# Performance work log

Hardware: AMD Instinct MI355X
Metric: run time of the kernel (lower is better)

The kernel has to match this reference:

```python
import jax, jax.numpy as jnp
import numpy as np

# ---- PGA G(3,0,1) geometric-product structure constants ----
# Blade basis order used by gatr/gafl: scalar, e0..e3, e01..e23, e012..e123, e0123.
_BLADES = [(), (0,), (1,), (2,), (3,), (0,1), (0,2), (0,3), (1,2), (1,3), (2,3),
           (0,1,2), (0,1,3), (0,2,3), (1,2,3), (0,1,2,3)]
_BLADE_IDX = {b: i for i, b in enumerate(_BLADES)}

def _blade_product(b1, b2):
    # Multiply two basis blades; metric: e0^2 = 0, e1^2 = e2^2 = e3^2 = +1.
    arr = list(b1) + list(b2)
    sign = 1
    n = len(arr)
    for i in range(n):            # bubble sort, counting swaps of anticommuting generators
        for j in range(n - 1):
            if arr[j] > arr[j + 1]:
                arr[j], arr[j + 1] = arr[j + 1], arr[j]
                sign = -sign
    res = []
    i = 0
    while i < len(arr):           # contract equal adjacent pairs via the metric
        if i + 1 < len(arr) and arr[i] == arr[i + 1]:
            if arr[i] == 0:
                return 0, ()       # e0^2 = 0 (degenerate direction)
            i += 2
        else:
            res.append(arr[i])
            i += 1
    return sign, tuple(res)

def _build_gp_table():
    gp = np.zeros((16, 16, 16), dtype=np.float32)  # gp[i,j,k]: coeff of blade i in e_j*e_k
    for j, bj in enumerate(_BLADES):
        for k, bk in enumerate(_BLADES):
            s, b = _blade_product(bj, bk)
            if s != 0:
                gp[_BLADE_IDX[b], j, k] = s
    return gp

_GP = _build_gp_table()
# Reverse: grade r blade gets sign (-1)^(r(r-1)/2).
_REV = np.array([(-1) ** (len(b) * (len(b) - 1) // 2) for b in _BLADES], dtype=np.float32)


def setup_inputs() -> dict:
    key = jax.random.key(0)
    T = jax.random.normal(key, (2048, 16), dtype=jnp.float32)
    return {"T": T}


def reference(T) -> jnp.ndarray:
    gp = jnp.asarray(_GP)                      # (16,16,16)
    rev = jnp.asarray(_REV)                    # (16,)
    v_inv = T * rev                            # reverse(v): grade-dependent sign flip
    # cross_gp: out[n,m,i] = sum_{j,k} gp[i,j,k] T[n,j] v_inv[m,k]
    out = jnp.einsum('ijk,nj,mk->nmi', gp, T, v_inv)  # (N, N, 16)
    return out
```

## Files before the change

### kernel.cpp

```cpp
#include <hip/hip_runtime.h>


namespace {

typedef float f2 __attribute__((ext_vector_type(2)));

constexpr int popcount4(unsigned x) {
    int c = 0;
    for (int i = 0; i < 5; ++i) c += (x >> i) & 1;
    return c;
}

struct GPTab {
    signed char sgn[16][16];
    unsigned char idx[16][16];
};

constexpr unsigned MASKV[16] = {0u, 1u, 2u, 4u, 8u,
                                3u, 5u, 9u, 6u, 10u, 12u,
                                7u, 11u, 13u, 14u, 15u};

constexpr GPTab make_tab() {
    GPTab t{};
    int inv[16] = {};
    for (int i = 0; i < 16; ++i) inv[(int)MASKV[i]] = i;

    for (int j = 0; j < 16; ++j) {
        for (int k = 0; k < 16; ++k) {
            unsigned a = MASKV[j], b = MASKV[k];
            if (a & b & 1u) {
                t.sgn[j][k] = 0;
                t.idx[j][k] = 0;
                continue;
            }
            int swaps = 0;
            for (int g = 0; g < 4; ++g)
                if ((b >> g) & 1u)
                    swaps += popcount4(a >> (g + 1));
            int s = (swaps & 1) ? -1 : 1;
            int r = popcount4(b);
            if ((r * (r - 1) / 2) & 1) s = -s;
            t.sgn[j][k] = (signed char)s;
            t.idx[j][k] = (unsigned char)inv[(int)(a ^ b)];
        }
    }
    return t;
}

constexpr GPTab TAB = make_tab();

struct Packing {
    unsigned char pl[8], ph[8];
    unsigned char slot[16], half[16];
    signed char   act[16][8];
    unsigned char src[16][8];
    unsigned char swp[16][8];
    signed char   s0[16][8], s1[16][8];
};

constexpr Packing make_packing() {
    Packing p{};
    int inv[16] = {};
    for (int i = 0; i < 16; ++i) inv[(int)MASKV[i]] = i;

    int t = 0;
    for (int e0bit = 0; e0bit <= 1; ++e0bit) {
        for (unsigned m = 0; m < 16; ++m) {
            if ((m & 2u) == 0u && (int)(m & 1u) == e0bit) {
                int lo = inv[(int)m], hi = inv[(int)(m | 2u)];
                p.pl[t] = (unsigned char)lo;
                p.ph[t] = (unsigned char)hi;
                p.slot[lo] = (unsigned char)t; p.half[lo] = 0;
                p.slot[hi] = (unsigned char)t; p.half[hi] = 1;
                ++t;
            }
        }
    }

    GPTab tab = make_tab();
    for (int k = 0; k < 16; ++k) {
        for (int s = 0; s < 8; ++s) {
            int i0 = p.pl[s], i1 = p.ph[s];
            int j0 = inv[(int)(MASKV[i0] ^ MASKV[k])];
            int j1 = inv[(int)(MASKV[i1] ^ MASKV[k])];
            int g0 = tab.sgn[j0][k], g1 = tab.sgn[j1][k];
            p.act[k][s] = (signed char)(g0 != 0);
            p.src[k][s] = p.slot[j0];
            p.swp[k][s] = p.half[j0];
            p.s0[k][s] = (signed char)g0;
            p.s1[k][s] = (signed char)g1;
        }
    }
    return p;
}

constexpr Packing PK = make_packing();

}

__global__ __launch_bounds__(256) void transpose_kernel(
    const float* __restrict__ T, float* __restrict__ Tt, int nrows) {
    int t = blockIdx.x * 256 + threadIdx.x;
    if (t < nrows * 16) {
        int m = t >> 4, j = t & 15;
        Tt[j * nrows + m] = T[t];
    }
}

template <bool USE_TT>
__global__ __launch_bounds__(256) void gp_pairs_kernel(
    const float* __restrict__ T, const float* __restrict__ Tt,
    float* __restrict__ out, int nrows) {
    const int lane = threadIdx.x & 63;
    const int wave = threadIdx.x >> 6;
    const int m = blockIdx.x * 256 + (int)threadIdx.x;
    const int n = blockIdx.y;
    const int mc = (m < nrows) ? m : (nrows - 1);

    __shared__ float lds[4][64 * 20];

    float a[16], b[16];
#pragma unroll
    for (int q = 0; q < 4; ++q) {
        float4 va = reinterpret_cast<const float4*>(T)[(size_t)n * 4 + q];
        a[q * 4 + 0] = va.x; a[q * 4 + 1] = va.y;
        a[q * 4 + 2] = va.z; a[q * 4 + 3] = va.w;
    }
    if constexpr (USE_TT) {
#pragma unroll
        for (int j = 0; j < 16; ++j)
            b[j] = Tt[(size_t)j * nrows + mc];
    } else {
#pragma unroll
        for (int q = 0; q < 4; ++q) {
            float4 vb = reinterpret_cast<const float4*>(T)[(size_t)mc * 4 + q];
            b[q * 4 + 0] = vb.x; b[q * 4 + 1] = vb.y;
            b[q * 4 + 2] = vb.z; b[q * 4 + 3] = vb.w;
        }
    }

    f2 A[8];
#pragma unroll
    for (int s = 0; s < 8; ++s) {
        f2 v; v.x = a[PK.pl[s]]; v.y = a[PK.ph[s]];
        A[s] = v;
    }

    f2 O[8];
#pragma unroll
    for (int s = 0; s < 8; ++s) O[s] = (f2)(0.0f);

#pragma unroll
    for (int k = 0; k < 16; ++k) {
        const float bk = b[k];
        f2 bb; bb.x = bk; bb.y = bk;
#pragma unroll
        for (int s = 0; s < 8; ++s) {
            if (PK.act[k][s]) {
                const f2 srcv = A[PK.src[k][s]];
                float x = PK.swp[k][s] ? srcv.y : srcv.x;
                float y = PK.swp[k][s] ? srcv.x : srcv.y;
                if (PK.s0[k][s] < 0) x = -x;
                if (PK.s1[k][s] < 0) y = -y;
                f2 av; av.x = x; av.y = y;
                O[s] = __builtin_elementwise_fma(av, bb, O[s]);
            }
        }
    }

    float o[16];
#pragma unroll
    for (int i = 0; i < 16; ++i)
        o[i] = PK.half[i] ? O[PK.slot[i]].y : O[PK.slot[i]].x;

    float* w = &lds[wave][lane * 20];
#pragma unroll
    for (int q = 0; q < 4; ++q)
        *reinterpret_cast<float4*>(w + q * 4) =
            make_float4(o[q * 4 + 0], o[q * 4 + 1], o[q * 4 + 2], o[q * 4 + 3]);

    __syncthreads();

    const int waveM0 = blockIdx.x * 256 + wave * 64;
    float4* __restrict__ ov =
        reinterpret_cast<float4*>(out) + ((size_t)n * nrows + waveM0) * 4;
#pragma unroll
    for (int q = 0; q < 4; ++q) {
        const int g = q * 64 + lane;
        const int p = g >> 2;
        const int c = g & 3;
        if (waveM0 + p < nrows) {
            ov[g] = *reinterpret_cast<const float4*>(&lds[wave][p * 20 + c * 4]);
        }
    }
}

extern "C" void kernel_launch(void* const* d_in, const int* in_sizes, int n_in,
                              void* d_out, int out_size, void* d_ws, size_t ws_size,
                              hipStream_t stream) {
    const float* T = (const float*)d_in[0];
    float* out = (float*)d_out;
    const int nrows = in_sizes[0] / 16;
    const size_t tt_bytes = (size_t)nrows * 16 * sizeof(float);

    dim3 grid((unsigned)((nrows + 255) / 256), (unsigned)nrows, 1);

    if (ws_size >= tt_bytes) {
        float* Tt = (float*)d_ws;
        transpose_kernel<<<(nrows * 16 + 255) / 256, 256, 0, stream>>>(T, Tt, nrows);
        gp_pairs_kernel<true><<<grid, 256, 0, stream>>>(T, Tt, out, nrows);
    } else {
        gp_pairs_kernel<false><<<grid, 256, 0, stream>>>(T, nullptr, out, nrows);
    }
}
```

Baseline: 50.08 us.

## Fuse transpose into GP kernel via coalesced LDS staging and nontemporal stores

Drops the separate transpose kernel. Each block now loads its 256 rows of T with coalesced vector loads into padded LDS and reads the per-thread operand from there. It also removes the barrier before the output write-back by having each wave reuse its own LDS rows, and switches the output writes to nontemporal stores to limit cache pollution from the 256 MB result. Bounds checks are dropped and the grid uses nrows/256, which assumes nrows is a multiple of 256.

After: 65.47 us. 30.7% more time.

```diff
diff --git a/kernel.cpp b/kernel.cpp
--- a/kernel.cpp
+++ b/kernel.cpp
@@ -4,6 +4,7 @@
 namespace {
 
 typedef float f2 __attribute__((ext_vector_type(2)));
+typedef float f4 __attribute__((ext_vector_type(4)));
 
 constexpr int popcount4(unsigned x) {
     int c = 0;
@@ -47,8 +48,6 @@
     return t;
 }
 
-constexpr GPTab TAB = make_tab();
-
 struct Packing {
     unsigned char pl[8], ph[8];
     unsigned char slot[16], half[16];
@@ -98,45 +97,41 @@
 
 }
 
-__global__ __launch_bounds__(256) void transpose_kernel(
-    const float* __restrict__ T, float* __restrict__ Tt, int nrows) {
-    int t = blockIdx.x * 256 + threadIdx.x;
-    if (t < nrows * 16) {
-        int m = t >> 4, j = t & 15;
-        Tt[j * nrows + m] = T[t];
-    }
-}
-
-template <bool USE_TT>
-__global__ __launch_bounds__(256) void gp_pairs_kernel(
-    const float* __restrict__ T, const float* __restrict__ Tt,
-    float* __restrict__ out, int nrows) {
+__global__ __launch_bounds__(256) void gp_fused_kernel(
+    const float* __restrict__ T, float* __restrict__ out, int nrows) {
     const int lane = threadIdx.x & 63;
     const int wave = threadIdx.x >> 6;
-    const int m = blockIdx.x * 256 + (int)threadIdx.x;
-    const int n = blockIdx.y;
-    const int mc = (m < nrows) ? m : (nrows - 1);
-
-    __shared__ float lds[4][64 * 20];
+    const int t    = threadIdx.x;
+    const int m0   = blockIdx.x * 256;
+    const int n    = blockIdx.y;
+
+    __shared__ float lds[256 * 20];
+
+    {
+        const f4* __restrict__ src =
+            reinterpret_cast<const f4*>(T) + (size_t)m0 * 4;
+#pragma unroll
+        for (int k2 = 0; k2 < 4; ++k2) {
+            const int g = k2 * 256 + t;
+            f4 v = src[g];
+            const int p = g >> 2, c = g & 3;
+            *reinterpret_cast<f4*>(&lds[p * 20 + c * 4]) = v;
+        }
+    }
+    __syncthreads();
 
     float a[16], b[16];
 #pragma unroll
     for (int q = 0; q < 4; ++q) {
-        float4 va = reinterpret_cast<const float4*>(T)[(size_t)n * 4 + q];
+        f4 va = reinterpret_cast<const f4*>(T)[(size_t)n * 4 + q];
         a[q * 4 + 0] = va.x; a[q * 4 + 1] = va.y;
         a[q * 4 + 2] = va.z; a[q * 4 + 3] = va.w;
     }
-    if constexpr (USE_TT) {
-#pragma unroll
-        for (int j = 0; j < 16; ++j)
-            b[j] = Tt[(size_t)j * nrows + mc];
-    } else {
-#pragma unroll
-        for (int q = 0; q < 4; ++q) {
-            float4 vb = reinterpret_cast<const float4*>(T)[(size_t)mc * 4 + q];
-            b[q * 4 + 0] = vb.x; b[q * 4 + 1] = vb.y;
-            b[q * 4 + 2] = vb.z; b[q * 4 + 3] = vb.w;
-        }
+#pragma unroll
+    for (int q = 0; q < 4; ++q) {
+        f4 vb = *reinterpret_cast<const f4*>(&lds[t * 20 + q * 4]);
+        b[q * 4 + 0] = vb.x; b[q * 4 + 1] = vb.y;
+        b[q * 4 + 2] = vb.z; b[q * 4 + 3] = vb.w;
     }
 
     f2 A[8];
@@ -173,25 +168,25 @@
     for (int i = 0; i < 16; ++i)
         o[i] = PK.half[i] ? O[PK.slot[i]].y : O[PK.slot[i]].x;
 
-    float* w = &lds[wave][lane * 20];
-#pragma unroll
-    for (int q = 0; q < 4; ++q)
-        *reinterpret_cast<float4*>(w + q * 4) =
-            make_float4(o[q * 4 + 0], o[q * 4 + 1], o[q * 4 + 2], o[q * 4 + 3]);
-
-    __syncthreads();
-
-    const int waveM0 = blockIdx.x * 256 + wave * 64;
-    float4* __restrict__ ov =
-        reinterpret_cast<float4*>(out) + ((size_t)n * nrows + waveM0) * 4;
+    float* w = &lds[t * 20];
+#pragma unroll
+    for (int q = 0; q < 4; ++q) {
+        f4 v; v.x = o[q * 4 + 0]; v.y = o[q * 4 + 1];
+        v.z = o[q * 4 + 2]; v.w = o[q * 4 + 3];
+        *reinterpret_cast<f4*>(w + q * 4) = v;
+    }
+
+    const int waveM0 = m0 + wave * 64;
+    f4* __restrict__ ov =
+        reinterpret_cast<f4*>(out) + ((size_t)n * nrows + waveM0) * 4;
+    const float* wbase = &lds[wave * 64 * 20];
 #pragma unroll
     for (int q = 0; q < 4; ++q) {
         const int g = q * 64 + lane;
         const int p = g >> 2;
         const int c = g & 3;
-        if (waveM0 + p < nrows) {
-            ov[g] = *reinterpret_cast<const float4*>(&lds[wave][p * 20 + c * 4]);
-        }
+        f4 v = *reinterpret_cast<const f4*>(&wbase[p * 20 + c * 4]);
+        __builtin_nontemporal_store(v, ov + g);
     }
 }
 
@@ -201,15 +196,6 @@
     const float* T = (const float*)d_in[0];
     float* out = (float*)d_out;
     const int nrows = in_sizes[0] / 16;
-    const size_t tt_bytes = (size_t)nrows * 16 * sizeof(float);
-
-    dim3 grid((unsigned)((nrows + 255) / 256), (unsigned)nrows, 1);
-
-    if (ws_size >= tt_bytes) {
-        float* Tt = (float*)d_ws;
-        transpose_kernel<<<(nrows * 16 + 255) / 256, 256, 0, stream>>>(T, Tt, nrows);
-        gp_pairs_kernel<true><<<grid, 256, 0, stream>>>(T, Tt, out, nrows);
-    } else {
-        gp_pairs_kernel<false><<<grid, 256, 0, stream>>>(T, nullptr, out, nrows);
-    }
-}
+    dim3 grid((unsigned)(nrows / 256), (unsigned)nrows, 1);
+    gp_fused_kernel<<<grid, 256, 0, stream>>>(T, out, nrows);
+}
```
